# Kernel optimization log

Hardware: AMD Instinct MI355X
Metric: run time of the kernel (lower is better)

Reference implementation:

```python
import jax, jax.numpy as jnp
import numpy as np

DIM = 2048
N_HEADS = 32
N_KV_HEADS = 8
HEAD_DIM = 64
REPEATS = N_HEADS // N_KV_HEADS
SCALE = HEAD_DIM ** -0.5
L = 2048
B = 1


def rotary_matrix(context_len, d):
    # Dense (L, d, d) RoPE rotation matrix, exactly as get_rotary_matrix1.
    pos = jnp.arange(1, context_len + 1, dtype=jnp.float32)[:, None]
    i = jnp.arange(d // 2)
    theta = 10000.0 ** (-2.0 * i.astype(jnp.float32) / d)
    m_theta = pos * theta  # (L, d/2)
    cos_v, sin_v = jnp.cos(m_theta), jnp.sin(m_theta)
    R = jnp.zeros((context_len, d, d), dtype=jnp.float32)
    R = R.at[:, 2 * i, 2 * i].set(cos_v)
    R = R.at[:, 2 * i, 2 * i + 1].set(-sin_v)
    R = R.at[:, 2 * i + 1, 2 * i].set(sin_v)
    R = R.at[:, 2 * i + 1, 2 * i + 1].set(cos_v)
    return R


def causal_mask(context_len):
    idx = jnp.arange(context_len)
    return (idx[:, None] < idx[None, :]).astype(jnp.float32) * -1e9


def setup_inputs() -> dict:
    key = jax.random.key(0)
    ks = jax.random.split(key, 5)
    x = jax.random.normal(ks[0], (B, L, DIM), dtype=jnp.float32)
    mask = causal_mask(L)
    wq_w = jax.random.normal(ks[1], (N_HEADS * HEAD_DIM, DIM), dtype=jnp.float32) * 0.02
    wk_w = jax.random.normal(ks[2], (N_KV_HEADS * HEAD_DIM, DIM), dtype=jnp.float32) * 0.02
    wv_w = jax.random.normal(ks[3], (N_KV_HEADS * HEAD_DIM, DIM), dtype=jnp.float32) * 0.02
    wo_w = jax.random.normal(ks[4], (DIM, N_HEADS * HEAD_DIM), dtype=jnp.float32) * 0.02
    return {"x": x, "mask": mask, "wq_w": wq_w, "wk_w": wk_w, "wv_w": wv_w, "wo_w": wo_w}


def reference(x, mask, wq_w, wk_w, wv_w, wo_w):
    Bx, Lx, D = x.shape
    # projections (torch Linear: y = x @ W.T)
    q = jnp.einsum('bld,od->blo', x, wq_w).reshape(Bx, Lx, N_HEADS, HEAD_DIM).transpose(0, 2, 1, 3)
    k = jnp.einsum('bld,od->blo', x, wk_w).reshape(Bx, Lx, N_KV_HEADS, HEAD_DIM).transpose(0, 2, 1, 3)
    v = jnp.einsum('bld,od->blo', x, wv_w).reshape(Bx, Lx, N_KV_HEADS, HEAD_DIM).transpose(0, 2, 1, 3)
    # GQA repeat of kv heads (interleaved, matching concat-unsqueeze-reshape)
    k = jnp.repeat(k, REPEATS, axis=1)
    v = jnp.repeat(v, REPEATS, axis=1)
    # dense-matrix RoPE on q and (repeated) k
    R = rotary_matrix(Lx, HEAD_DIM)
    q = jnp.einsum('bhlj,lij->bhli', q, R)
    k = jnp.einsum('bhlj,lij->bhli', k, R)
    scores = jnp.einsum('bhld,bhmd->bhlm', q, k) * SCALE + mask
    attn = jax.nn.softmax(scores.astype(jnp.float32), axis=-1)
    out = jnp.einsum('bhlm,bhmd->bhld', attn, v)
    out = out.transpose(0, 2, 1, 3).reshape(Bx, Lx, N_HEADS * HEAD_DIM)
    out = jnp.einsum('blo,do->bld', out, wo_w)
    return out, k, v
```

## Files before the change

kernel.cpp:

```cpp
#include <hip/hip_runtime.h>

typedef __bf16 bf16;
typedef __bf16 bf16x8 __attribute__((ext_vector_type(8)));
typedef float floatx4 __attribute__((ext_vector_type(4)));
typedef float floatx16 __attribute__((ext_vector_type(16)));
typedef unsigned int uint;

#define MFMA16(a, b, c) __builtin_amdgcn_mfma_f32_16x16x32_bf16((a), (b), (c), 0, 0, 0)
#define MFMA32(a, b, c) __builtin_amdgcn_mfma_f32_32x32x16_bf16((a), (b), (c), 0, 0, 0)

__device__ __forceinline__ void gl2lds16(const bf16* g, bf16* l) {
  __builtin_amdgcn_global_load_lds(
      (const __attribute__((address_space(1))) void*)g,
      (__attribute__((address_space(3))) void*)l, 16, 0, 0);
}
__device__ __forceinline__ void wait_vm0() { __builtin_amdgcn_s_waitcnt(0x0f70); }

__device__ __forceinline__ void cvt8(const float* __restrict__ s,
                                     bf16* __restrict__ d, int i8) {
  const float4 a = ((const float4*)s)[i8 * 2];
  const float4 b = ((const float4*)s)[i8 * 2 + 1];
  bf16x8 o;
  o[0] = (bf16)a.x; o[1] = (bf16)a.y; o[2] = (bf16)a.z; o[3] = (bf16)a.w;
  o[4] = (bf16)b.x; o[5] = (bf16)b.y; o[6] = (bf16)b.z; o[7] = (bf16)b.w;
  *(bf16x8*)(d + i8 * 8) = o;
}

__global__ __launch_bounds__(256) void convert_kernel(
    const float* __restrict__ x, const float* __restrict__ wq,
    const float* __restrict__ wk, const float* __restrict__ wv,
    const float* __restrict__ wo, bf16* __restrict__ xb,
    bf16* __restrict__ wqb, bf16* __restrict__ wkb, bf16* __restrict__ wvb,
    bf16* __restrict__ wob) {
  const int g = blockIdx.x * 256 + threadIdx.x;
  if (g < 524288) cvt8(x, xb, g);
  else if (g < 1048576) cvt8(wq, wqb, g - 524288);
  else if (g < 1179648) cvt8(wk, wkb, g - 1048576);
  else if (g < 1310720) cvt8(wv, wvb, g - 1179648);
  else cvt8(wo, wob, g - 1310720);
}

template <typename OutT>
__device__ __forceinline__ void gemm_tile_body(
    const bf16* __restrict__ A, int lda,
    const bf16* __restrict__ B, int ldb,
    OutT* __restrict__ C, int ldc, int K,
    bf16* As, bf16* Bs) {
  const int t = threadIdx.x;
  const int w = t >> 6, lane = t & 63;
  const int l15 = lane & 15, qd = lane >> 4;
  const int wr = w >> 1, wc = w & 1;

  floatx4 acc[4][4];
#pragma unroll
  for (int i = 0; i < 4; ++i)
#pragma unroll
    for (int j = 0; j < 4; ++j) acc[i][j] = (floatx4){0.f, 0.f, 0.f, 0.f};

  const int mt0 = w, mt1 = w + 4;
  const int kseg = qd * 8;
  const bf16* ga0 = A + (mt0 * 16 + l15) * lda + kseg;
  const bf16* ga1 = A + (mt1 * 16 + l15) * lda + kseg;
  const bf16* gb0 = B + (mt0 * 16 + l15) * ldb + kseg;
  const bf16* gb1 = B + (mt1 * 16 + l15) * ldb + kseg;
  bf16* lA0 = As + mt0 * 512 + lane * 8;
  bf16* lA1 = As + mt1 * 512 + lane * 8;
  bf16* lB0 = Bs + mt0 * 512 + lane * 8;
  bf16* lB1 = Bs + mt1 * 512 + lane * 8;

  for (int k0 = 0; k0 < K; k0 += 32) {
    gl2lds16(ga0 + k0, lA0);
    gl2lds16(ga1 + k0, lA1);
    gl2lds16(gb0 + k0, lB0);
    gl2lds16(gb1 + k0, lB1);
    wait_vm0();
    __syncthreads();

    bf16x8 a[4], b[4];
#pragma unroll
    for (int i = 0; i < 4; ++i)
      a[i] = *(const bf16x8*)(As + (wr * 4 + i) * 512 + lane * 8);
#pragma unroll
    for (int j = 0; j < 4; ++j)
      b[j] = *(const bf16x8*)(Bs + (wc * 4 + j) * 512 + lane * 8);
#pragma unroll
    for (int i = 0; i < 4; ++i)
#pragma unroll
      for (int j = 0; j < 4; ++j) acc[i][j] = MFMA16(a[i], b[j], acc[i][j]);
    __syncthreads();
  }

#pragma unroll
  for (int i = 0; i < 4; ++i)
#pragma unroll
    for (int j = 0; j < 4; ++j) {
      const int row = wr * 64 + i * 16 + qd * 4;
      const int col = wc * 64 + j * 16 + l15;
#pragma unroll
      for (int r = 0; r < 4; ++r)
        C[(row + r) * ldc + col] = (OutT)acc[i][j][r];
    }
}

__global__ __launch_bounds__(256) void gemm_qkv(
    const bf16* __restrict__ x, const bf16* __restrict__ wq,
    const bf16* __restrict__ wk, const bf16* __restrict__ wv,
    bf16* __restrict__ Qws, bf16* __restrict__ Kws, bf16* __restrict__ Vws) {
  __shared__ bf16 As[4096], Bs[4096];
  const int m0 = blockIdx.y * 128;
  const int nb = blockIdx.x;
  const bf16* B;
  bf16* C;
  int ldc;
  if (nb < 16) {
    B = wq + nb * 128 * 2048;
    C = Qws + m0 * 2048 + nb * 128;
    ldc = 2048;
  } else if (nb < 20) {
    B = wk + (nb - 16) * 128 * 2048;
    C = Kws + m0 * 512 + (nb - 16) * 128;
    ldc = 512;
  } else {
    B = wv + (nb - 20) * 128 * 2048;
    C = Vws + m0 * 512 + (nb - 20) * 128;
    ldc = 512;
  }
  gemm_tile_body<bf16>(x + m0 * 2048, 2048, B, 2048, C, ldc, 2048, As, Bs);
}

__global__ __launch_bounds__(256) void gemm_o(
    const bf16* __restrict__ Ows, const bf16* __restrict__ wo,
    float* __restrict__ out) {
  __shared__ bf16 As[4096], Bs[4096];
  const int m0 = blockIdx.y * 128, n0 = blockIdx.x * 128;
  gemm_tile_body<float>(Ows + m0 * 2048, 2048, wo + n0 * 2048, 2048,
                        out + m0 * 2048 + n0, 2048, 2048, As, Bs);
}

__global__ __launch_bounds__(256) void rope_repeat_kernel(
    bf16* __restrict__ Qws, bf16* __restrict__ Kws, bf16* __restrict__ Kh,
    const bf16* __restrict__ Vws, bf16* __restrict__ Vt,
    float* __restrict__ kout, float* __restrict__ vout) {
  const int gid = blockIdx.x * 256 + threadIdx.x;
  const float NEG_LOG2_10000_D32 = -0.4152410118609203f;
  if (gid < 2097152) {
    const int l = gid >> 10, pr = gid & 1023, a = pr & 31;
    bf16* p = Qws + l * 2048 + pr * 2;
    const float x0 = (float)p[0], x1 = (float)p[1];
    const float ang = (float)(l + 1) * exp2f(NEG_LOG2_10000_D32 * (float)a);
    float s, c;
    __sincosf(ang, &s, &c);
    p[0] = (bf16)(c * x0 - s * x1);
    p[1] = (bf16)(s * x0 + c * x1);
  } else if (gid < 2097152 + 524288) {
    const int g = gid - 2097152;
    const int l = g >> 8, pr = g & 255, a = pr & 31, kvh = pr >> 5;
    bf16* p = Kws + l * 512 + pr * 2;
    const float x0 = (float)p[0], x1 = (float)p[1];
    const float ang = (float)(l + 1) * exp2f(NEG_LOG2_10000_D32 * (float)a);
    float s, c;
    __sincosf(ang, &s, &c);
    const float y0 = c * x0 - s * x1;
    const float y1 = s * x0 + c * x1;
    p[0] = (bf16)y0;
    p[1] = (bf16)y1;
    bf16* kp = Kh + (kvh * 2048 + l) * 64 + a * 2;
    kp[0] = (bf16)y0;
    kp[1] = (bf16)y1;
#pragma unroll
    for (int rep = 0; rep < 4; ++rep) {
      float* o = kout + (((kvh * 4 + rep) * 2048 + l) * 64 + a * 2);
      o[0] = y0;
      o[1] = y1;
    }
  } else if (gid < 2097152 + 524288 + 131072) {
    const int c = gid - (2097152 + 524288);
    const int l = c >> 6, seg = c & 63, kvh = seg >> 3;
    const bf16x8 v = *(const bf16x8*)(Vws + l * 512 + seg * 8);
    float4 f0, f1;
    f0.x = (float)v[0]; f0.y = (float)v[1]; f0.z = (float)v[2]; f0.w = (float)v[3];
    f1.x = (float)v[4]; f1.y = (float)v[5]; f1.z = (float)v[6]; f1.w = (float)v[7];
#pragma unroll
    for (int rep = 0; rep < 4; ++rep) {
      float* o = vout + (((kvh * 4 + rep) * 2048 + l) * 64 + (seg & 7) * 8);
      *(float4*)o = f0;
      *(float4*)(o + 4) = f1;
    }
  } else {
    const int c = gid - (2097152 + 524288 + 131072);
    const int kvh = c >> 14, r2 = c & 16383, dseg = r2 >> 11, l = r2 & 2047;
    const int d0 = dseg * 8;
    const bf16x8 v = *(const bf16x8*)(Vws + l * 512 + kvh * 64 + d0);
#pragma unroll
    for (int jj = 0; jj < 8; ++jj)
      Vt[kvh * 131072 + (d0 + jj) * 2048 + l] = v[jj];
  }
}

__global__ __launch_bounds__(256) void flash_kernel(
    const bf16* __restrict__ Qws, const bf16* __restrict__ Kh,
    const bf16* __restrict__ Vt, bf16* __restrict__ Ows) {
  __shared__ bf16 KVs[2][2][4096];
  __shared__ bf16 Osh[128 * 66];

  const int h = blockIdx.y;
  const int qt = ((h >> 4) & 1) ? (int)blockIdx.x : 15 - (int)blockIdx.x;
  const int kh = h >> 2;
  const int q0 = qt * 128;
  const int t = threadIdx.x, w = t >> 6, lane = t & 63;
  const int l31 = lane & 31, hf = lane >> 5;
  const int qw = q0 + w * 32;

  bf16x8 qf[4];
  {
    const bf16* qrow = Qws + (qw + l31) * 2048 + h * 64 + hf * 8;
#pragma unroll
    for (int c = 0; c < 4; ++c) qf[c] = *(const bf16x8*)(qrow + c * 16);
  }

  floatx16 o[2] = {};
  float mrun = -3e38f, lrun = 0.f;

  const int s0 = w, s1 = w + 4;
  const bf16* gK0 = Kh + kh * 131072 + ((s0 >> 2) * 32 + l31) * 64 + (s0 & 3) * 16 + hf * 8;
  const bf16* gK1 = Kh + kh * 131072 + ((s1 >> 2) * 32 + l31) * 64 + (s1 & 3) * 16 + hf * 8;
  const bf16* gV0 = Vt + kh * 131072 + ((s0 >> 2) * 32 + l31) * 2048 + (s0 & 3) * 16 + hf * 8;
  const bf16* gV1 = Vt + kh * 131072 + ((s1 >> 2) * 32 + l31) * 2048 + (s1 & 3) * 16 + hf * 8;

  const int nkt = 2 * qt + 2;
  gl2lds16(gK0, &KVs[0][0][s0 * 512 + lane * 8]);
  gl2lds16(gK1, &KVs[0][0][s1 * 512 + lane * 8]);
  gl2lds16(gV0, &KVs[0][1][s0 * 512 + lane * 8]);
  gl2lds16(gV1, &KVs[0][1][s1 * 512 + lane * 8]);

  const float C = 0.1803368801f;
  for (int kt = 0; kt < nkt; ++kt) {
    wait_vm0();
    __syncthreads();
    if (kt + 1 < nkt) {
      const int nb = (kt + 1) & 1;
      const int koff = (kt + 1) * 4096, voff = (kt + 1) * 64;
      gl2lds16(gK0 + koff, &KVs[nb][0][s0 * 512 + lane * 8]);
      gl2lds16(gK1 + koff, &KVs[nb][0][s1 * 512 + lane * 8]);
      gl2lds16(gV0 + voff, &KVs[nb][1][s0 * 512 + lane * 8]);
      gl2lds16(gV1 + voff, &KVs[nb][1][s1 * 512 + lane * 8]);
    }
    const int kt64 = kt * 64;
    if (kt64 > qw + 31) continue;
    const bf16* Kb = &KVs[kt & 1][0][0];
    const bf16* Vb = &KVs[kt & 1][1][0];

    floatx16 st[2];
#pragma unroll
    for (int tt = 0; tt < 2; ++tt) {
      floatx16 z = {};
#pragma unroll
      for (int c = 0; c < 4; ++c) {
        const bf16x8 kf = *(const bf16x8*)(Kb + (tt * 4 + c) * 512 + lane * 8);
        z = MFMA32(kf, qf[c], z);
      }
      st[tt] = z;
    }
    if (kt64 + 64 > qw) {
      const int myq = qw + l31;
#pragma unroll
      for (int tt = 0; tt < 2; ++tt)
#pragma unroll
        for (int r = 0; r < 16; ++r) {
          const int key = kt64 + tt * 32 + (r & 3) + 8 * (r >> 2) + 4 * hf;
          if (key > myq) st[tt][r] = -1e30f;
        }
    }
    float mx = -3e38f;
#pragma unroll
    for (int tt = 0; tt < 2; ++tt)
#pragma unroll
      for (int r = 0; r < 16; ++r) mx = fmaxf(mx, st[tt][r]);
    mx = fmaxf(mx, __shfl_xor(mx, 32));
    const float mn = fmaxf(mrun, mx);
    const float al = __builtin_amdgcn_exp2f((mrun - mn) * C);
    mrun = mn;
    float rs = 0.f;
#pragma unroll
    for (int tt = 0; tt < 2; ++tt)
#pragma unroll
      for (int r = 0; r < 16; ++r) {
        const float p = __builtin_amdgcn_exp2f((st[tt][r] - mn) * C);
        st[tt][r] = p;
        rs += p;
      }
    rs += __shfl_xor(rs, 32);
    lrun = lrun * al + rs;
#pragma unroll
    for (int n = 0; n < 2; ++n)
#pragma unroll
      for (int r = 0; r < 16; ++r) o[n][r] *= al;

    uint pk[2][4][2];
#pragma unroll
    for (int tt = 0; tt < 2; ++tt)
#pragma unroll
      for (int g = 0; g < 4; ++g)
#pragma unroll
        for (int p = 0; p < 2; ++p) {
          union { bf16 h2[2]; uint u; } cv;
          cv.h2[0] = (bf16)st[tt][4 * g + 2 * p];
          cv.h2[1] = (bf16)st[tt][4 * g + 2 * p + 1];
          pk[tt][g][p] = cv.u;
        }
    uint own_[2][2][2], rv[2][2][2];
#pragma unroll
    for (int tt = 0; tt < 2; ++tt)
#pragma unroll
      for (int gam = 0; gam < 2; ++gam)
#pragma unroll
        for (int p = 0; p < 2; ++p) {
          own_[tt][gam][p] = hf ? pk[tt][2 * gam + 1][p] : pk[tt][2 * gam][p];
          const uint snd = hf ? pk[tt][2 * gam][p] : pk[tt][2 * gam + 1][p];
          rv[tt][gam][p] = (uint)__shfl_xor((int)snd, 32);
        }
#pragma unroll
    for (int c = 0; c < 4; ++c) {
      const int tt = c >> 1, gam = c & 1;
      union { uint u[4]; bf16x8 v; } pf;
      pf.u[0] = hf ? rv[tt][gam][0] : own_[tt][gam][0];
      pf.u[1] = hf ? rv[tt][gam][1] : own_[tt][gam][1];
      pf.u[2] = hf ? own_[tt][gam][0] : rv[tt][gam][0];
      pf.u[3] = hf ? own_[tt][gam][1] : rv[tt][gam][1];
#pragma unroll
      for (int n = 0; n < 2; ++n)
        o[n] = MFMA32(*(const bf16x8*)(Vb + (n * 4 + c) * 512 + lane * 8),
                      pf.v, o[n]);
    }
  }

  const float inv = 1.f / lrun;
#pragma unroll
  for (int n = 0; n < 2; ++n)
#pragma unroll
    for (int r = 0; r < 16; ++r) {
      const int dl = n * 32 + (r & 3) + 8 * (r >> 2) + 4 * hf;
      Osh[(w * 32 + l31) * 66 + dl] = (bf16)(o[n][r] * inv);
    }
  __syncthreads();
#pragma unroll
  for (int i = 0; i < 4; ++i) {
    const int row = (t >> 3) + i * 32;
    const int col = (t & 7) * 8;
    const bf16x8 vv = *(const bf16x8*)&Osh[row * 66 + col];
    *(bf16x8*)&Ows[(q0 + row) * 2048 + h * 64 + col] = vv;
  }
}

extern "C" void kernel_launch(void* const* d_in, const int* in_sizes, int n_in,
                              void* d_out, int out_size, void* d_ws,
                              size_t ws_size, hipStream_t stream) {
  const float* x = (const float*)d_in[0];
  const float* wq = (const float*)d_in[2];
  const float* wk = (const float*)d_in[3];
  const float* wv = (const float*)d_in[4];
  const float* wo = (const float*)d_in[5];

  float* out = (float*)d_out;
  float* kout = out + 4194304;
  float* vout = out + 8388608;

  bf16* ws = (bf16*)d_ws;
  bf16* xb = ws;
  bf16* wqb = xb + 4194304;
  bf16* wkb = wqb + 4194304;
  bf16* wvb = wkb + 1048576;
  bf16* wob = wvb + 1048576;
  bf16* Qws = wob + 4194304;
  bf16* Kws = Qws + 4194304;
  bf16* Vws = Kws + 1048576;
  bf16* Vt = Vws + 1048576;
  bf16* Ows = Vt + 1048576;
  bf16* Kh = Ows + 4194304;

  convert_kernel<<<dim3(7168), dim3(256), 0, stream>>>(x, wq, wk, wv, wo, xb,
                                                       wqb, wkb, wvb, wob);
  gemm_qkv<<<dim3(24, 16), dim3(256), 0, stream>>>(xb, wqb, wkb, wvb, Qws, Kws,
                                                   Vws);
  rope_repeat_kernel<<<dim3(11264), dim3(256), 0, stream>>>(Qws, Kws, Kh, Vws,
                                                            Vt, kout, vout);
  flash_kernel<<<dim3(16, 32), dim3(256), 0, stream>>>(Qws, Kh, Vt, Ows);
  gemm_o<<<dim3(16, 16), dim3(256), 0, stream>>>(Ows, wob, out);
}
```

Before: 314.3 us.

## Split long causal query tiles across two KV segments with combine kernel

Query tiles 8-15 are split into two blocks, each covering half of the KV range. Each writes unnormalized fp32 partial outputs plus running max and sum to scratch, and a new combine kernel merges them into bf16 output. The scratch reuses the output buffer and the K workspace. The aim is to balance causal work across more blocks. The change also adds lazy rescaling that skips the O rescale when the max grows by less than a threshold, s_setprio around the MFMA sections, and split accumulators for the max and sum reductions. The cost is an extra kernel launch and the fp32 partial traffic.

```diff
diff --git a/kernel.cpp b/kernel.cpp
--- a/kernel.cpp
+++ b/kernel.cpp
@@ -199,12 +199,24 @@
 
 __global__ __launch_bounds__(256) void flash_kernel(
     const bf16* __restrict__ Qws, const bf16* __restrict__ Kh,
-    const bf16* __restrict__ Vt, bf16* __restrict__ Ows) {
+    const bf16* __restrict__ Vt, bf16* __restrict__ Ows,
+    float* __restrict__ Opart, float* __restrict__ ML) {
   __shared__ bf16 KVs[2][2][4096];
   __shared__ bf16 Osh[128 * 66];
 
   const int h = blockIdx.y;
-  const int qt = ((h >> 4) & 1) ? (int)blockIdx.x : 15 - (int)blockIdx.x;
+  const int bx = blockIdx.x;
+  int qt, seg, kts, kte;
+  if (bx < 8) {
+    qt = bx; seg = -1; kts = 0; kte = 2 * qt + 2;
+  } else {
+    const int i = bx - 8;
+    qt = 8 + (i >> 1);
+    seg = i & 1;
+    const int half = qt + 1;
+    kts = seg * half;
+    kte = kts + half;
+  }
   const int kh = h >> 2;
   const int q0 = qt * 128;
   const int t = threadIdx.x, w = t >> 6, lane = t & 63;
@@ -227,17 +239,19 @@
   const bf16* gV0 = Vt + kh * 131072 + ((s0 >> 2) * 32 + l31) * 2048 + (s0 & 3) * 16 + hf * 8;
   const bf16* gV1 = Vt + kh * 131072 + ((s1 >> 2) * 32 + l31) * 2048 + (s1 & 3) * 16 + hf * 8;
 
-  const int nkt = 2 * qt + 2;
-  gl2lds16(gK0, &KVs[0][0][s0 * 512 + lane * 8]);
-  gl2lds16(gK1, &KVs[0][0][s1 * 512 + lane * 8]);
-  gl2lds16(gV0, &KVs[0][1][s0 * 512 + lane * 8]);
-  gl2lds16(gV1, &KVs[0][1][s1 * 512 + lane * 8]);
+  {
+    const int nb = kts & 1;
+    gl2lds16(gK0 + kts * 4096, &KVs[nb][0][s0 * 512 + lane * 8]);
+    gl2lds16(gK1 + kts * 4096, &KVs[nb][0][s1 * 512 + lane * 8]);
+    gl2lds16(gV0 + kts * 64, &KVs[nb][1][s0 * 512 + lane * 8]);
+    gl2lds16(gV1 + kts * 64, &KVs[nb][1][s1 * 512 + lane * 8]);
+  }
 
   const float C = 0.1803368801f;
-  for (int kt = 0; kt < nkt; ++kt) {
+  for (int kt = kts; kt < kte; ++kt) {
     wait_vm0();
     __syncthreads();
-    if (kt + 1 < nkt) {
+    if (kt + 1 < kte) {
       const int nb = (kt + 1) & 1;
       const int koff = (kt + 1) * 4096, voff = (kt + 1) * 64;
       gl2lds16(gK0 + koff, &KVs[nb][0][s0 * 512 + lane * 8]);
@@ -251,6 +265,7 @@
     const bf16* Vb = &KVs[kt & 1][1][0];
 
     floatx16 st[2];
+    __builtin_amdgcn_s_setprio(1);
 #pragma unroll
     for (int tt = 0; tt < 2; ++tt) {
       floatx16 z = {};
@@ -261,6 +276,7 @@
       }
       st[tt] = z;
     }
+    __builtin_amdgcn_s_setprio(0);
     if (kt64 + 64 > qw) {
       const int myq = qw + l31;
 #pragma unroll
@@ -271,30 +287,46 @@
           if (key > myq) st[tt][r] = -1e30f;
         }
     }
-    float mx = -3e38f;
+    float ma = -3e38f, mb = -3e38f, mc = -3e38f, md = -3e38f;
 #pragma unroll
     for (int tt = 0; tt < 2; ++tt)
 #pragma unroll
-      for (int r = 0; r < 16; ++r) mx = fmaxf(mx, st[tt][r]);
+      for (int r = 0; r < 16; r += 4) {
+        ma = fmaxf(ma, st[tt][r + 0]);
+        mb = fmaxf(mb, st[tt][r + 1]);
+        mc = fmaxf(mc, st[tt][r + 2]);
+        md = fmaxf(md, st[tt][r + 3]);
+      }
+    float mx = fmaxf(fmaxf(ma, mb), fmaxf(mc, md));
     mx = fmaxf(mx, __shfl_xor(mx, 32));
-    const float mn = fmaxf(mrun, mx);
-    const float al = __builtin_amdgcn_exp2f((mrun - mn) * C);
-    mrun = mn;
-    float rs = 0.f;
+    const bool defer = __all((mx - mrun) * C <= 8.f);
+    if (!defer) {
+      const float mn = fmaxf(mrun, mx);
+      const float al = __builtin_amdgcn_exp2f((mrun - mn) * C);
+      lrun *= al;
+#pragma unroll
+      for (int n = 0; n < 2; ++n)
+#pragma unroll
+        for (int r = 0; r < 16; ++r) o[n][r] *= al;
+      mrun = mn;
+    }
+    float ra = 0.f, rb = 0.f, rc = 0.f, rd = 0.f;
 #pragma unroll
     for (int tt = 0; tt < 2; ++tt)
 #pragma unroll
-      for (int r = 0; r < 16; ++r) {
-        const float p = __builtin_amdgcn_exp2f((st[tt][r] - mn) * C);
-        st[tt][r] = p;
-        rs += p;
+      for (int r = 0; r < 16; r += 4) {
+        const float p0 = __builtin_amdgcn_exp2f((st[tt][r + 0] - mrun) * C);
+        const float p1 = __builtin_amdgcn_exp2f((st[tt][r + 1] - mrun) * C);
+        const float p2 = __builtin_amdgcn_exp2f((st[tt][r + 2] - mrun) * C);
+        const float p3 = __builtin_amdgcn_exp2f((st[tt][r + 3] - mrun) * C);
+        st[tt][r + 0] = p0; ra += p0;
+        st[tt][r + 1] = p1; rb += p1;
+        st[tt][r + 2] = p2; rc += p2;
+        st[tt][r + 3] = p3; rd += p3;
       }
+    float rs = (ra + rb) + (rc + rd);
     rs += __shfl_xor(rs, 32);
-    lrun = lrun * al + rs;
-#pragma unroll
-    for (int n = 0; n < 2; ++n)
-#pragma unroll
-      for (int r = 0; r < 16; ++r) o[n][r] *= al;
+    lrun += rs;
 
     uint pk[2][4][2];
 #pragma unroll
@@ -319,6 +351,7 @@
           const uint snd = hf ? pk[tt][2 * gam][p] : pk[tt][2 * gam + 1][p];
           rv[tt][gam][p] = (uint)__shfl_xor((int)snd, 32);
         }
+    __builtin_amdgcn_s_setprio(1);
 #pragma unroll
     for (int c = 0; c < 4; ++c) {
       const int tt = c >> 1, gam = c & 1;
@@ -332,23 +365,75 @@
         o[n] = MFMA32(*(const bf16x8*)(Vb + (n * 4 + c) * 512 + lane * 8),
                       pf.v, o[n]);
     }
-  }
-
-  const float inv = 1.f / lrun;
-#pragma unroll
-  for (int n = 0; n < 2; ++n)
-#pragma unroll
-    for (int r = 0; r < 16; ++r) {
-      const int dl = n * 32 + (r & 3) + 8 * (r >> 2) + 4 * hf;
-      Osh[(w * 32 + l31) * 66 + dl] = (bf16)(o[n][r] * inv);
-    }
+    __builtin_amdgcn_s_setprio(0);
+  }
+
+  if (seg < 0) {
+    const float inv = 1.f / lrun;
+#pragma unroll
+    for (int n = 0; n < 2; ++n)
+#pragma unroll
+      for (int r = 0; r < 16; ++r) {
+        const int dl = n * 32 + (r & 3) + 8 * (r >> 2) + 4 * hf;
+        Osh[(w * 32 + l31) * 66 + dl] = (bf16)(o[n][r] * inv);
+      }
+    __syncthreads();
+#pragma unroll
+    for (int i = 0; i < 4; ++i) {
+      const int row = (t >> 3) + i * 32;
+      const int col = (t & 7) * 8;
+      const bf16x8 vv = *(const bf16x8*)&Osh[row * 66 + col];
+      *(bf16x8*)&Ows[(q0 + row) * 2048 + h * 64 + col] = vv;
+    }
+  } else {
+    const int idx = (h * 8 + (qt - 8)) * 2 + seg;
+    float* Op = Opart + idx * 8192;
+#pragma unroll
+    for (int n = 0; n < 2; ++n)
+#pragma unroll
+      for (int r = 0; r < 16; ++r) {
+        const int dl = n * 32 + (r & 3) + 8 * (r >> 2) + 4 * hf;
+        Op[dl * 128 + w * 32 + l31] = o[n][r];
+      }
+    if (hf == 0) {
+      ML[idx * 256 + w * 32 + l31] = mrun;
+      ML[idx * 256 + 128 + w * 32 + l31] = lrun;
+    }
+  }
+}
+
+__global__ __launch_bounds__(256) void combine_kernel(
+    const float* __restrict__ Opart, const float* __restrict__ ML,
+    bf16* __restrict__ Ows) {
+  __shared__ bf16 Osh[128 * 66];
+  const int b = blockIdx.x;
+  const int h = b >> 3, qt = (b & 7) + 8;
+  const int q0 = qt * 128;
+  const int t = threadIdx.x;
+  const int row = t & 127, dh = t >> 7;
+  const int i0 = (h * 8 + (qt - 8)) * 2;
+  const float C = 0.1803368801f;
+  const float m0 = ML[i0 * 256 + row], l0 = ML[i0 * 256 + 128 + row];
+  const float m1 = ML[(i0 + 1) * 256 + row], l1 = ML[(i0 + 1) * 256 + 128 + row];
+  const float m = fmaxf(m0, m1);
+  const float w0 = __builtin_amdgcn_exp2f((m0 - m) * C);
+  const float w1 = __builtin_amdgcn_exp2f((m1 - m) * C);
+  const float inv = 1.f / (l0 * w0 + l1 * w1);
+  const float* P0 = Opart + i0 * 8192;
+  const float* P1 = Opart + (i0 + 1) * 8192;
+#pragma unroll
+  for (int j = 0; j < 32; ++j) {
+    const int d = dh * 32 + j;
+    const float v = (P0[d * 128 + row] * w0 + P1[d * 128 + row] * w1) * inv;
+    Osh[row * 66 + d] = (bf16)v;
+  }
   __syncthreads();
 #pragma unroll
   for (int i = 0; i < 4; ++i) {
-    const int row = (t >> 3) + i * 32;
+    const int r2 = (t >> 3) + i * 32;
     const int col = (t & 7) * 8;
-    const bf16x8 vv = *(const bf16x8*)&Osh[row * 66 + col];
-    *(bf16x8*)&Ows[(q0 + row) * 2048 + h * 64 + col] = vv;
+    const bf16x8 vv = *(const bf16x8*)&Osh[r2 * 66 + col];
+    *(bf16x8*)&Ows[(q0 + r2) * 2048 + h * 64 + col] = vv;
   }
 }
 
@@ -377,6 +462,8 @@
   bf16* Vt = Vws + 1048576;
   bf16* Ows = Vt + 1048576;
   bf16* Kh = Ows + 4194304;
+  float* Opart = out;
+  float* MLf = (float*)Kws;
 
   convert_kernel<<<dim3(7168), dim3(256), 0, stream>>>(x, wq, wk, wv, wo, xb,
                                                        wqb, wkb, wvb, wob);
@@ -384,6 +471,8 @@
                                                    Vws);
   rope_repeat_kernel<<<dim3(11264), dim3(256), 0, stream>>>(Qws, Kws, Kh, Vws,
                                                             Vt, kout, vout);
-  flash_kernel<<<dim3(16, 32), dim3(256), 0, stream>>>(Qws, Kh, Vt, Ows);
+  flash_kernel<<<dim3(24, 32), dim3(256), 0, stream>>>(Qws, Kh, Vt, Ows, Opart,
+                                                       MLf);
+  combine_kernel<<<dim3(256), dim3(256), 0, stream>>>(Opart, MLf, Ows);
   gemm_o<<<dim3(16, 16), dim3(256), 0, stream>>>(Ows, wob, out);
 }
```

Result: faster. 307.7 us (-2.1%).
